# Kernel tuning notes

Measured on AMD Instinct MI355X. Metric: run time of the kernel, lower is better.

## Reference

```python
import jax, jax.numpy as jnp
import numpy as np

IN_F, OUT_F, GROUP = 4096, 11008, 128

# NF4 codebook (normalized-float-4 levels), matches NF4_LEVELS in the source
NF4_LEVELS = jnp.array([
    -1.0, -0.6961928009986877, -0.5250730514526367, -0.39491748809814453,
    -0.28444138169288635, -0.18477343022823334, -0.09105003625154495, 0.0,
    0.07958029955625534, 0.16093020141124725, 0.24611230194568634,
    0.33791524171829224, 0.44070982933044434, 0.5626170039176941,
    0.7229568362236023, 1.0], dtype=jnp.float32)


def setup_inputs() -> dict:
    key = jax.random.key(0)
    k0, k1, k2, k3 = jax.random.split(key, 4)
    x = jax.random.normal(k0, (32, 1, IN_F), dtype=jnp.float32)
    # one int32 per packed byte; low nibble = even element code, high nibble = odd
    packed = jax.random.randint(k1, (OUT_F * IN_F // 2,), 0, 256, dtype=jnp.int32)
    # per-group absmax scales (positive)
    scales = jax.random.uniform(k2, (OUT_F * IN_F // GROUP,), dtype=jnp.float32) * 0.02 + 1e-4
    bias_param = jax.random.normal(k3, (OUT_F,), dtype=jnp.float32)
    return {"x": x, "packed": packed, "scales": scales, "bias_param": bias_param}


def dequant_nf4(packed, scales):
    # unpack two 4-bit codes per byte; interleave as quantized[0::2]=low, [1::2]=high
    low = packed & 15
    high = (packed >> 4) & 15
    codes = jnp.stack([low, high], axis=-1).reshape(-1)          # [OUT_F*IN_F]
    vals = NF4_LEVELS[codes]                                      # codebook lookup
    w = (vals.reshape(-1, GROUP) * scales[:, None]).reshape(OUT_F, IN_F)
    return w


def reference(x, packed, scales, bias_param):
    W = dequant_nf4(packed, scales)                               # [OUT_F, IN_F]
    # y = x @ W^T + b  (F.linear semantics)
    return jnp.einsum('bsi,oi->bso', x, W) + bias_param
```

## Files before the change

### kernel.cpp

```cpp
#include <hip/hip_runtime.h>
#include <hip/hip_bf16.h>

#define IN_F   4096
#define OUT_F  11008
#define BATCH  32
#define GROUP  128
#define NTILE  16
#define KSPLIT 4
#define GRID_N (OUT_F / NTILE)
#define OUTSZ  (BATCH * OUT_F)

typedef __attribute__((ext_vector_type(8))) short  bf16x8;
typedef __attribute__((ext_vector_type(4))) float  f32x4;
typedef __attribute__((ext_vector_type(4))) int    i32x4;
typedef __attribute__((ext_vector_type(4))) float  float4v;

static __device__ __constant__ float NF4_LEVELS[16] = {
    -1.0f, -0.6961928009986877f, -0.5250730514526367f, -0.39491748809814453f,
    -0.28444138169288635f, -0.18477343022823334f, -0.09105003625154495f, 0.0f,
    0.07958029955625534f, 0.16093020141124725f, 0.24611230194568634f,
    0.33791524171829224f, 0.44070982933044434f, 0.5626170039176941f,
    0.7229568362236023f, 1.0f};

__global__ void prelude_kernel(const float* __restrict__ x,
                               const float* __restrict__ bias,
                               unsigned short* __restrict__ frag,
                               float* __restrict__ out) {
    const int bid = blockIdx.x, tid = threadIdx.x;
    if (bid < 64) {
        int T  = bid * 256 + tid;
        int st = T >> 13;
        int kb = (T >> 6) & 127;
        int l  = T & 63;
        int row = st * 16 + (l & 15);
        int k0  = kb * 32 + (l >> 4) * 8;
        const float* src = x + (size_t)row * IN_F + k0;
        unsigned w[4];
        #pragma unroll
        for (int e = 0; e < 4; ++e) {
            unsigned lo = __builtin_bit_cast(unsigned short, __float2bfloat16(src[2 * e]));
            unsigned hi = __builtin_bit_cast(unsigned short, __float2bfloat16(src[2 * e + 1]));
            w[e] = lo | (hi << 16);
        }
        i32x4 v = { (int)w[0], (int)w[1], (int)w[2], (int)w[3] };
        *reinterpret_cast<i32x4*>(frag + ((size_t)st * 8192 + kb * 64 + l) * 8) = v;
    } else {
        int t2 = (bid - 64) * 256 + tid;
        int i  = t2 * 4;
        int o  = i % OUT_F;
        float4v b = *reinterpret_cast<const float4v*>(bias + o);
        *reinterpret_cast<float4v*>(out + i) = b;
    }
}

__global__ __launch_bounds__(256, 8) void nf4_gemm_kernel(
        const int* __restrict__ packed,
        const float* __restrict__ scales,
        const unsigned short* __restrict__ frag,
        float* __restrict__ out)
{
    __shared__ unsigned tabu[256];
    __shared__ float    slds[512];
    __shared__ unsigned buf[2][1024];

    const int tid  = threadIdx.x;
    const int wave = tid >> 6;
    const int lane = tid & 63;
    const int col  = lane & 15;
    const int g    = lane >> 4;

    {
        unsigned lo = __builtin_bit_cast(unsigned short, __float2bfloat16(NF4_LEVELS[tid & 15]));
        unsigned hi = __builtin_bit_cast(unsigned short, __float2bfloat16(NF4_LEVELS[(tid >> 4) & 15]));
        tabu[tid] = lo | (hi << 16);
    }

    const int n0 = blockIdx.x * NTILE;

    {
        int e = tid * 2;
        float2 sv = *reinterpret_cast<const float2*>(scales + (size_t)n0 * 32 + e);
        int c0 = e >> 5, g0 = e & 31;
        slds[g0 * 16 + c0]       = sv.x;
        slds[(g0 + 1) * 16 + c0] = sv.y;
    }

    const int kint0 = blockIdx.y * 512;
    const int kbB   = blockIdx.y * 32;
    const int grB   = blockIdx.y * 8;
    const int dperm = (lane & 0x30) | ((lane & 3) << 2) | ((lane >> 2) & 3);

    #define PLOAD(u, sr)                                                       \
        _Pragma("unroll")                                                      \
        for (int ii = 0; ii < 4; ++ii) {                                       \
            sr[ii] = *reinterpret_cast<const i32x4*>(                          \
                packed + (size_t)(n0 + wave * 4 + ii) * (IN_F / 2)             \
                       + kint0 + (u) * 256 + lane * 4);                        \
        }

    #define PWRITE(u, sr)                                                      \
        _Pragma("unroll")                                                      \
        for (int ii = 0; ii < 4; ++ii) {                                       \
            int row = wave * 4 + ii;                                           \
            unsigned v = ((unsigned)(sr[ii][0] & 255))                         \
                       | ((unsigned)(sr[ii][1] & 255) << 8)                    \
                       | ((unsigned)(sr[ii][2] & 255) << 16)                   \
                       | ((unsigned)(sr[ii][3] & 255) << 24);                  \
            buf[(u) & 1][(row * 64 + dperm) ^ ((row & 7) << 2)] = v;           \
        }

    i32x4 sB[4];
    {
        i32x4 sA[4];
        PLOAD(0, sA)
        PLOAD(1, sB)
        PWRITE(0, sA)
    }
    __syncthreads();

    f32x4 acc0 = (f32x4){0.f,0.f,0.f,0.f};
    f32x4 acc1 = (f32x4){0.f,0.f,0.f,0.f};

    const unsigned short* f0 = frag;
    const unsigned short* f1 = frag + 65536;

    #pragma unroll
    for (int u = 0; u < 2; ++u) {
        bf16x8 A0[4], A1[4];
        #pragma unroll
        for (int t = 0; t < 4; ++t) {
            int kb = kbB + u * 16 + wave * 4 + t;
            A0[t] = *reinterpret_cast<const bf16x8*>(f0 + ((size_t)kb * 64 + lane) * 8);
            A1[t] = *reinterpret_cast<const bf16x8*>(f1 + ((size_t)kb * 64 + lane) * 8);
        }

        i32x4 cdv = *reinterpret_cast<const i32x4*>(
            &buf[u & 1][(col * 64 + wave * 16 + g * 4) ^ ((col & 7) << 2)]);
        float sc = slds[(grB + u * 4 + wave) * 16 + col];

        f32x4 t0 = (f32x4){0.f,0.f,0.f,0.f};
        f32x4 t1 = (f32x4){0.f,0.f,0.f,0.f};
        #pragma unroll
        for (int t = 0; t < 4; ++t) {
            unsigned code = (unsigned)cdv[t];
            i32x4 bu;
            bu[0] = (int)tabu[code & 255u];
            bu[1] = (int)tabu[(code >> 8) & 255u];
            bu[2] = (int)tabu[(code >> 16) & 255u];
            bu[3] = (int)tabu[code >> 24];
            bf16x8 bf = __builtin_bit_cast(bf16x8, bu);
            t0 = __builtin_amdgcn_mfma_f32_16x16x32_bf16(A0[t], bf, t0, 0, 0, 0);
            t1 = __builtin_amdgcn_mfma_f32_16x16x32_bf16(A1[t], bf, t1, 0, 0, 0);
        }
        #pragma unroll
        for (int j = 0; j < 4; ++j) {
            acc0[j] = fmaf(sc, t0[j], acc0[j]);
            acc1[j] = fmaf(sc, t1[j], acc1[j]);
        }

        if (u == 0) { PWRITE(1, sB) }
        __syncthreads();
    }

    float* red = (float*)buf;
    #pragma unroll
    for (int j = 0; j < 4; ++j) {
        red[wave * 512 + j * 64 + lane]       = acc0[j];
        red[wave * 512 + (4 + j) * 64 + lane] = acc1[j];
    }
    __syncthreads();

    #pragma unroll
    for (int p = 0; p < 2; ++p) {
        int idx = p * 256 + tid;
        int b   = idx >> 4;
        int c   = idx & 15;
        int h   = b >> 4;
        int r4  = b & 15;
        int j   = r4 & 3;
        int lg  = r4 >> 2;
        int slot = (h * 4 + j) * 64 + lg * 16 + c;
        float s = red[slot] + red[512 + slot] + red[1024 + slot] + red[1536 + slot];
        unsafeAtomicAdd(out + (size_t)b * OUT_F + n0 + c, s);
    }
}

extern "C" void kernel_launch(void* const* d_in, const int* in_sizes, int n_in,
                              void* d_out, int out_size, void* d_ws, size_t ws_size,
                              hipStream_t stream) {
    const float* x      = (const float*)d_in[0];
    const int*   packed = (const int*)d_in[1];
    const float* scales = (const float*)d_in[2];
    const float* bias   = (const float*)d_in[3];
    float* out = (float*)d_out;

    unsigned short* frag = (unsigned short*)d_ws;

    prelude_kernel<<<408, 256, 0, stream>>>(x, bias, frag, out);
    nf4_gemm_kernel<<<dim3(GRID_N, KSPLIT), 256, 0, stream>>>(packed, scales, frag, out);
}
```

Baseline: 28.61 us.

## Widen N tile to 32 and split K eight ways with single-stage blocks

Each block now covers 32 output columns and one 512-wide K slice (KSPLIT 8). Every block loads its packed weights and activation fragments once, so the two-stage double-buffered loop is gone. Each activation fragment load now feeds two N subtiles, which halves activation reuse traffic per weight byte. In exchange there are twice as many atomic adds to the output, each block holds more registers and LDS (launch bounds lowered to 6), and there is no overlap between loads and compute inside a block.

```diff
diff --git a/kernel.cpp b/kernel.cpp
--- a/kernel.cpp
+++ b/kernel.cpp
@@ -5,8 +5,8 @@
 #define OUT_F  11008
 #define BATCH  32
 #define GROUP  128
-#define NTILE  16
-#define KSPLIT 4
+#define NTILE  32
+#define KSPLIT 8
 #define GRID_N (OUT_F / NTILE)
 #define OUTSZ  (BATCH * OUT_F)
 
@@ -53,15 +53,15 @@
     }
 }
 
-__global__ __launch_bounds__(256, 8) void nf4_gemm_kernel(
+__global__ __launch_bounds__(256, 6) void nf4_gemm_kernel(
         const int* __restrict__ packed,
         const float* __restrict__ scales,
         const unsigned short* __restrict__ frag,
         float* __restrict__ out)
 {
     __shared__ unsigned tabu[256];
-    __shared__ float    slds[512];
-    __shared__ unsigned buf[2][1024];
+    __shared__ float    slds[128];
+    __shared__ unsigned lds[4096];
 
     const int tid  = threadIdx.x;
     const int wave = tid >> 6;
@@ -76,112 +76,105 @@
     }
 
     const int n0 = blockIdx.x * NTILE;
+    const int by = blockIdx.y;
 
-    {
-        int e = tid * 2;
-        float2 sv = *reinterpret_cast<const float2*>(scales + (size_t)n0 * 32 + e);
-        int c0 = e >> 5, g0 = e & 31;
-        slds[g0 * 16 + c0]       = sv.x;
-        slds[(g0 + 1) * 16 + c0] = sv.y;
+    if (tid < 128) {
+        int w = tid >> 5, r = tid & 31;
+        slds[w * 32 + r] = scales[(size_t)(n0 + r) * 32 + by * 4 + w];
     }
 
-    const int kint0 = blockIdx.y * 512;
-    const int kbB   = blockIdx.y * 32;
-    const int grB   = blockIdx.y * 8;
     const int dperm = (lane & 0x30) | ((lane & 3) << 2) | ((lane >> 2) & 3);
 
-    #define PLOAD(u, sr)                                                       \
-        _Pragma("unroll")                                                      \
-        for (int ii = 0; ii < 4; ++ii) {                                       \
-            sr[ii] = *reinterpret_cast<const i32x4*>(                          \
-                packed + (size_t)(n0 + wave * 4 + ii) * (IN_F / 2)             \
-                       + kint0 + (u) * 256 + lane * 4);                        \
-        }
+    i32x4 sr[8];
+    #pragma unroll
+    for (int ii = 0; ii < 8; ++ii) {
+        int row = wave * 8 + ii;
+        sr[ii] = *reinterpret_cast<const i32x4*>(
+            packed + (size_t)(n0 + row) * (IN_F / 2) + by * 256 + lane * 4);
+    }
 
-    #define PWRITE(u, sr)                                                      \
-        _Pragma("unroll")                                                      \
-        for (int ii = 0; ii < 4; ++ii) {                                       \
-            int row = wave * 4 + ii;                                           \
-            unsigned v = ((unsigned)(sr[ii][0] & 255))                         \
-                       | ((unsigned)(sr[ii][1] & 255) << 8)                    \
-                       | ((unsigned)(sr[ii][2] & 255) << 16)                   \
-                       | ((unsigned)(sr[ii][3] & 255) << 24);                  \
-            buf[(u) & 1][(row * 64 + dperm) ^ ((row & 7) << 2)] = v;           \
-        }
+    const unsigned short* f0 = frag;
+    const unsigned short* f1 = frag + 65536;
+    bf16x8 A0[4], A1[4];
+    #pragma unroll
+    for (int t = 0; t < 4; ++t) {
+        int kb = by * 16 + wave * 4 + t;
+        A0[t] = *reinterpret_cast<const bf16x8*>(f0 + ((size_t)kb * 64 + lane) * 8);
+        A1[t] = *reinterpret_cast<const bf16x8*>(f1 + ((size_t)kb * 64 + lane) * 8);
+    }
 
-    i32x4 sB[4];
-    {
-        i32x4 sA[4];
-        PLOAD(0, sA)
-        PLOAD(1, sB)
-        PWRITE(0, sA)
+    #pragma unroll
+    for (int ii = 0; ii < 8; ++ii) {
+        int row = wave * 8 + ii;
+        unsigned v = ((unsigned)(sr[ii][0] & 255))
+                   | ((unsigned)(sr[ii][1] & 255) << 8)
+                   | ((unsigned)(sr[ii][2] & 255) << 16)
+                   | ((unsigned)(sr[ii][3] & 255) << 24);
+        lds[(row * 64 + dperm) ^ ((row & 7) << 2)] = v;
     }
     __syncthreads();
 
-    f32x4 acc0 = (f32x4){0.f,0.f,0.f,0.f};
-    f32x4 acc1 = (f32x4){0.f,0.f,0.f,0.f};
+    i32x4 cd[2];
+    #pragma unroll
+    for (int st = 0; st < 2; ++st) {
+        int row = st * 16 + col;
+        cd[st] = *reinterpret_cast<const i32x4*>(
+            &lds[(row * 64 + wave * 16 + g * 4) ^ ((row & 7) << 2)]);
+    }
 
-    const unsigned short* f0 = frag;
-    const unsigned short* f1 = frag + 65536;
+    f32x4 t0[2], t1[2];
+    #pragma unroll
+    for (int st = 0; st < 2; ++st) {
+        t0[st] = (f32x4){0.f,0.f,0.f,0.f};
+        t1[st] = (f32x4){0.f,0.f,0.f,0.f};
+    }
 
     #pragma unroll
-    for (int u = 0; u < 2; ++u) {
-        bf16x8 A0[4], A1[4];
+    for (int t = 0; t < 4; ++t) {
         #pragma unroll
-        for (int t = 0; t < 4; ++t) {
-            int kb = kbB + u * 16 + wave * 4 + t;
-            A0[t] = *reinterpret_cast<const bf16x8*>(f0 + ((size_t)kb * 64 + lane) * 8);
-            A1[t] = *reinterpret_cast<const bf16x8*>(f1 + ((size_t)kb * 64 + lane) * 8);
-        }
-
-        i32x4 cdv = *reinterpret_cast<const i32x4*>(
-            &buf[u & 1][(col * 64 + wave * 16 + g * 4) ^ ((col & 7) << 2)]);
-        float sc = slds[(grB + u * 4 + wave) * 16 + col];
-
-        f32x4 t0 = (f32x4){0.f,0.f,0.f,0.f};
-        f32x4 t1 = (f32x4){0.f,0.f,0.f,0.f};
-        #pragma unroll
-        for (int t = 0; t < 4; ++t) {
-            unsigned code = (unsigned)cdv[t];
+        for (int st = 0; st < 2; ++st) {
+            unsigned code = (unsigned)cd[st][t];
             i32x4 bu;
             bu[0] = (int)tabu[code & 255u];
             bu[1] = (int)tabu[(code >> 8) & 255u];
             bu[2] = (int)tabu[(code >> 16) & 255u];
             bu[3] = (int)tabu[code >> 24];
             bf16x8 bf = __builtin_bit_cast(bf16x8, bu);
-            t0 = __builtin_amdgcn_mfma_f32_16x16x32_bf16(A0[t], bf, t0, 0, 0, 0);
-            t1 = __builtin_amdgcn_mfma_f32_16x16x32_bf16(A1[t], bf, t1, 0, 0, 0);
+            t0[st] = __builtin_amdgcn_mfma_f32_16x16x32_bf16(A0[t], bf, t0[st], 0, 0, 0);
+            t1[st] = __builtin_amdgcn_mfma_f32_16x16x32_bf16(A1[t], bf, t1[st], 0, 0, 0);
         }
+    }
+
+    float sc[2];
+    sc[0] = slds[wave * 32 + col];
+    sc[1] = slds[wave * 32 + 16 + col];
+
+    __syncthreads();
+
+    float* red = (float*)lds;
+    #pragma unroll
+    for (int st = 0; st < 2; ++st)
         #pragma unroll
         for (int j = 0; j < 4; ++j) {
-            acc0[j] = fmaf(sc, t0[j], acc0[j]);
-            acc1[j] = fmaf(sc, t1[j], acc1[j]);
+            red[wave * 1024 + (st * 2 + 0) * 256 + j * 64 + lane] = sc[st] * t0[st][j];
+            red[wave * 1024 + (st * 2 + 1) * 256 + j * 64 + lane] = sc[st] * t1[st][j];
         }
-
-        if (u == 0) { PWRITE(1, sB) }
-        __syncthreads();
-    }
-
-    float* red = (float*)buf;
-    #pragma unroll
-    for (int j = 0; j < 4; ++j) {
-        red[wave * 512 + j * 64 + lane]       = acc0[j];
-        red[wave * 512 + (4 + j) * 64 + lane] = acc1[j];
-    }
     __syncthreads();
 
     #pragma unroll
-    for (int p = 0; p < 2; ++p) {
+    for (int p = 0; p < 4; ++p) {
         int idx = p * 256 + tid;
-        int b   = idx >> 4;
-        int c   = idx & 15;
+        int o   = idx & 31;
+        int b   = idx >> 5;
+        int st  = o >> 4;
+        int c   = o & 15;
         int h   = b >> 4;
-        int r4  = b & 15;
-        int j   = r4 & 3;
-        int lg  = r4 >> 2;
-        int slot = (h * 4 + j) * 64 + lg * 16 + c;
-        float s = red[slot] + red[512 + slot] + red[1024 + slot] + red[1536 + slot];
-        unsafeAtomicAdd(out + (size_t)b * OUT_F + n0 + c, s);
+        int r   = b & 15;
+        int j   = r & 3;
+        int g2  = r >> 2;
+        int slot = (st * 2 + h) * 256 + j * 64 + g2 * 16 + c;
+        float s = red[slot] + red[1024 + slot] + red[2048 + slot] + red[3072 + slot];
+        unsafeAtomicAdd(out + (size_t)b * OUT_F + n0 + o, s);
     }
 }
 
```

Result: slower. 35.38 us (+23.6%).

## Widen N tile to 64 with per-wave private LDS staging and codebook

Applied to the files above, without the earlier changes.

Each block now covers 64 output columns instead of 16. Each wave owns a private K slice of packed codes, its own copy of the codebook table and reads its own scales from registers, so the main loop needs no block-level barriers. The A fragments loaded per wave are reused across four N subtiles, and the atomic epilogue now issues coalesced 64-wide rows. The trade-off is a 4x smaller grid (172x4 blocks), lower occupancy (launch bounds 4) and about 36KB of LDS per block.

```diff
diff --git a/kernel.cpp b/kernel.cpp
--- a/kernel.cpp
+++ b/kernel.cpp
@@ -4,11 +4,9 @@
 #define IN_F   4096
 #define OUT_F  11008
 #define BATCH  32
-#define GROUP  128
-#define NTILE  16
+#define NTILE  64
 #define KSPLIT 4
 #define GRID_N (OUT_F / NTILE)
-#define OUTSZ  (BATCH * OUT_F)
 
 typedef __attribute__((ext_vector_type(8))) short  bf16x8;
 typedef __attribute__((ext_vector_type(4))) float  f32x4;
@@ -53,15 +51,13 @@
     }
 }
 
-__global__ __launch_bounds__(256, 8) void nf4_gemm_kernel(
+__global__ __launch_bounds__(256, 4) void nf4_gemm_kernel(
         const int* __restrict__ packed,
         const float* __restrict__ scales,
         const unsigned short* __restrict__ frag,
         float* __restrict__ out)
 {
-    __shared__ unsigned tabu[256];
-    __shared__ float    slds[512];
-    __shared__ unsigned buf[2][1024];
+    __shared__ unsigned lds[9216];
 
     const int tid  = threadIdx.x;
     const int wave = tid >> 6;
@@ -69,119 +65,117 @@
     const int col  = lane & 15;
     const int g    = lane >> 4;
 
-    {
-        unsigned lo = __builtin_bit_cast(unsigned short, __float2bfloat16(NF4_LEVELS[tid & 15]));
-        unsigned hi = __builtin_bit_cast(unsigned short, __float2bfloat16(NF4_LEVELS[(tid >> 4) & 15]));
-        tabu[tid] = lo | (hi << 16);
+    const int n0 = blockIdx.x * NTILE;
+    const int by = blockIdx.y;
+
+    #pragma unroll
+    for (int q = 0; q < 4; ++q) {
+        int e = q * 64 + lane;
+        unsigned lo = __builtin_bit_cast(unsigned short, __float2bfloat16(NF4_LEVELS[e & 15]));
+        unsigned hi = __builtin_bit_cast(unsigned short, __float2bfloat16(NF4_LEVELS[(e >> 4) & 15]));
+        lds[wave * 256 + e] = lo | (hi << 16);
     }
 
-    const int n0 = blockIdx.x * NTILE;
+    float2 scp[4];
+    #pragma unroll
+    for (int st = 0; st < 4; ++st)
+        scp[st] = *reinterpret_cast<const float2*>(
+            scales + (size_t)(n0 + st * 16 + col) * 32 + by * 8 + wave * 2);
 
-    {
-        int e = tid * 2;
-        float2 sv = *reinterpret_cast<const float2*>(scales + (size_t)n0 * 32 + e);
-        int c0 = e >> 5, g0 = e & 31;
-        slds[g0 * 16 + c0]       = sv.x;
-        slds[(g0 + 1) * 16 + c0] = sv.y;
-    }
-
-    const int kint0 = blockIdx.y * 512;
-    const int kbB   = blockIdx.y * 32;
-    const int grB   = blockIdx.y * 8;
-    const int dperm = (lane & 0x30) | ((lane & 3) << 2) | ((lane >> 2) & 3);
-
-    #define PLOAD(u, sr)                                                       \
+    #define SLOAD(bb, sr)                                                      \
         _Pragma("unroll")                                                      \
-        for (int ii = 0; ii < 4; ++ii) {                                       \
+        for (int ii = 0; ii < 8; ++ii) {                                       \
+            int row = (bb) * 16 + 2 * ii + (lane >> 5);                        \
             sr[ii] = *reinterpret_cast<const i32x4*>(                          \
-                packed + (size_t)(n0 + wave * 4 + ii) * (IN_F / 2)             \
-                       + kint0 + (u) * 256 + lane * 4);                        \
+                packed + (size_t)(n0 + row) * (IN_F / 2)                       \
+                       + by * 512 + wave * 128 + (lane & 31) * 4);             \
         }
 
-    #define PWRITE(u, sr)                                                      \
+    #define SWRITE(bb, sr)                                                     \
         _Pragma("unroll")                                                      \
-        for (int ii = 0; ii < 4; ++ii) {                                       \
-            int row = wave * 4 + ii;                                           \
+        for (int ii = 0; ii < 8; ++ii) {                                       \
+            int row = (bb) * 16 + 2 * ii + (lane >> 5);                        \
+            int j   = lane & 31;                                               \
+            int d   = (j & 0x10) | ((j & 3) << 2) | ((j >> 2) & 3);            \
             unsigned v = ((unsigned)(sr[ii][0] & 255))                         \
                        | ((unsigned)(sr[ii][1] & 255) << 8)                    \
                        | ((unsigned)(sr[ii][2] & 255) << 16)                   \
                        | ((unsigned)(sr[ii][3] & 255) << 24);                  \
-            buf[(u) & 1][(row * 64 + dperm) ^ ((row & 7) << 2)] = v;           \
+            lds[1024 + wave * 2048 + ((row * 32 + d) ^ ((row & 7) << 2))] = v; \
         }
 
-    i32x4 sB[4];
     {
-        i32x4 sA[4];
-        PLOAD(0, sA)
-        PLOAD(1, sB)
-        PWRITE(0, sA)
+        i32x4 sa[8], sb[8];
+        SLOAD(0, sa) SLOAD(1, sb) SWRITE(0, sa)
+        SLOAD(2, sa) SWRITE(1, sb)
+        SLOAD(3, sb) SWRITE(2, sa) SWRITE(3, sb)
     }
-    __syncthreads();
 
-    f32x4 acc0 = (f32x4){0.f,0.f,0.f,0.f};
-    f32x4 acc1 = (f32x4){0.f,0.f,0.f,0.f};
+    f32x4 acc[4][2];
+    #pragma unroll
+    for (int st = 0; st < 4; ++st) {
+        acc[st][0] = (f32x4){0.f,0.f,0.f,0.f};
+        acc[st][1] = (f32x4){0.f,0.f,0.f,0.f};
+    }
 
     const unsigned short* f0 = frag;
     const unsigned short* f1 = frag + 65536;
 
     #pragma unroll
-    for (int u = 0; u < 2; ++u) {
+    for (int grp = 0; grp < 2; ++grp) {
         bf16x8 A0[4], A1[4];
         #pragma unroll
         for (int t = 0; t < 4; ++t) {
-            int kb = kbB + u * 16 + wave * 4 + t;
+            int kb = by * 32 + wave * 8 + grp * 4 + t;
             A0[t] = *reinterpret_cast<const bf16x8*>(f0 + ((size_t)kb * 64 + lane) * 8);
             A1[t] = *reinterpret_cast<const bf16x8*>(f1 + ((size_t)kb * 64 + lane) * 8);
         }
+        #pragma unroll
+        for (int st = 0; st < 4; ++st) {
+            int row = st * 16 + col;
+            i32x4 cd = *reinterpret_cast<const i32x4*>(
+                &lds[1024 + wave * 2048 +
+                     ((row * 32 + grp * 16 + g * 4) ^ ((row & 7) << 2))]);
+            f32x4 t0 = (f32x4){0.f,0.f,0.f,0.f};
+            f32x4 t1 = (f32x4){0.f,0.f,0.f,0.f};
+            #pragma unroll
+            for (int t = 0; t < 4; ++t) {
+                unsigned code = (unsigned)cd[t];
+                i32x4 bu;
+                bu[0] = (int)lds[wave * 256 + (code & 255u)];
+                bu[1] = (int)lds[wave * 256 + ((code >> 8) & 255u)];
+                bu[2] = (int)lds[wave * 256 + ((code >> 16) & 255u)];
+                bu[3] = (int)lds[wave * 256 + (code >> 24)];
+                bf16x8 bf = __builtin_bit_cast(bf16x8, bu);
+                t0 = __builtin_amdgcn_mfma_f32_16x16x32_bf16(A0[t], bf, t0, 0, 0, 0);
+                t1 = __builtin_amdgcn_mfma_f32_16x16x32_bf16(A1[t], bf, t1, 0, 0, 0);
+            }
+            const float sc = (grp == 0) ? scp[st].x : scp[st].y;
+            #pragma unroll
+            for (int j = 0; j < 4; ++j) {
+                acc[st][0][j] = fmaf(sc, t0[j], acc[st][0][j]);
+                acc[st][1][j] = fmaf(sc, t1[j], acc[st][1][j]);
+            }
+        }
+    }
 
-        i32x4 cdv = *reinterpret_cast<const i32x4*>(
-            &buf[u & 1][(col * 64 + wave * 16 + g * 4) ^ ((col & 7) << 2)]);
-        float sc = slds[(grB + u * 4 + wave) * 16 + col];
-
-        f32x4 t0 = (f32x4){0.f,0.f,0.f,0.f};
-        f32x4 t1 = (f32x4){0.f,0.f,0.f,0.f};
-        #pragma unroll
-        for (int t = 0; t < 4; ++t) {
-            unsigned code = (unsigned)cdv[t];
-            i32x4 bu;
-            bu[0] = (int)tabu[code & 255u];
-            bu[1] = (int)tabu[(code >> 8) & 255u];
-            bu[2] = (int)tabu[(code >> 16) & 255u];
-            bu[3] = (int)tabu[code >> 24];
-            bf16x8 bf = __builtin_bit_cast(bf16x8, bu);
-            t0 = __builtin_amdgcn_mfma_f32_16x16x32_bf16(A0[t], bf, t0, 0, 0, 0);
-            t1 = __builtin_amdgcn_mfma_f32_16x16x32_bf16(A1[t], bf, t1, 0, 0, 0);
-        }
+    float* red = (float*)&lds[1024 + wave * 2048];
+    #pragma unroll
+    for (int st = 0; st < 4; ++st)
         #pragma unroll
         for (int j = 0; j < 4; ++j) {
-            acc0[j] = fmaf(sc, t0[j], acc0[j]);
-            acc1[j] = fmaf(sc, t1[j], acc1[j]);
+            red[(0 * 16 + g * 4 + j) * 64 + st * 16 + col] = acc[st][0][j];
+            red[(1 * 16 + g * 4 + j) * 64 + st * 16 + col] = acc[st][1][j];
         }
-
-        if (u == 0) { PWRITE(1, sB) }
-        __syncthreads();
-    }
-
-    float* red = (float*)buf;
-    #pragma unroll
-    for (int j = 0; j < 4; ++j) {
-        red[wave * 512 + j * 64 + lane]       = acc0[j];
-        red[wave * 512 + (4 + j) * 64 + lane] = acc1[j];
-    }
     __syncthreads();
 
+    const float* rbase = (const float*)&lds[1024];
     #pragma unroll
-    for (int p = 0; p < 2; ++p) {
-        int idx = p * 256 + tid;
-        int b   = idx >> 4;
-        int c   = idx & 15;
-        int h   = b >> 4;
-        int r4  = b & 15;
-        int j   = r4 & 3;
-        int lg  = r4 >> 2;
-        int slot = (h * 4 + j) * 64 + lg * 16 + c;
-        float s = red[slot] + red[512 + slot] + red[1024 + slot] + red[1536 + slot];
-        unsafeAtomicAdd(out + (size_t)b * OUT_F + n0 + c, s);
+    for (int p = 0; p < 8; ++p) {
+        int b = p * 4 + wave;
+        float s = rbase[b * 64 + lane] + rbase[2048 + b * 64 + lane]
+                + rbase[4096 + b * 64 + lane] + rbase[6144 + b * 64 + lane];
+        unsafeAtomicAdd(out + (size_t)b * OUT_F + n0 + lane, s);
     }
 }
 
```

Measured after the change: 29.94 us. +4.7%, slower.
